# Kernel tuning notes

Hardware: AMD Instinct MI355X
Metric: run time of the kernel (lower is better)

The kernel has to match this reference:

```python
import jax, jax.numpy as jnp
import numpy as np

N_USERS = 50000
N_ITEMS = 100000
N_ENT = 200000
N_REL_TOTAL = 32  # n_relations * 2
DIM = 64
N_INTENTS = 2
N_LAYERS = 1
B = 4096
E_KG = 2_000_000
E_UI_HALF = 1_000_000  # user->item interactions; symmetrized to 2M directed edges


def setup_inputs() -> dict:
    key = jax.random.key(0)
    ks = jax.random.split(key, 16)
    s = 0.05  # xavier-ish scale
    user_emb = jax.random.normal(ks[0], (N_USERS, DIM), jnp.float32) * s
    entity_emb = jax.random.normal(ks[1], (N_ENT, DIM), jnp.float32) * s
    relation_emb = jax.random.normal(ks[2], (N_REL_TOTAL, DIM), jnp.float32) * s
    intent_weights = jax.random.normal(ks[3], (N_INTENTS, N_REL_TOTAL), jnp.float32) * s
    router_w = jax.random.normal(ks[4], (N_INTENTS, DIM), jnp.float32) * s
    router_b = jnp.zeros((N_INTENTS,), jnp.float32)
    kg_w = jax.random.normal(ks[5], (N_LAYERS, DIM, DIM), jnp.float32) * (1.0 / np.sqrt(DIM))
    item2entity = jax.random.randint(ks[6], (N_ITEMS,), 0, N_ENT)
    kg_src = jax.random.randint(ks[7], (E_KG,), 0, N_ENT)
    kg_dst = jax.random.randint(ks[8], (E_KG,), 0, N_ENT)
    kg_rel = jax.random.randint(ks[9], (E_KG,), 0, N_REL_TOTAL)
    # UI bipartite graph, symmetrically normalized (D^-1/2 A D^-1/2), as in _build_ui_graph
    rng = np.random.default_rng(0)
    uu = rng.integers(0, N_USERS, E_UI_HALF)
    ii = rng.integers(0, N_ITEMS, E_UI_HALF) + N_USERS
    rows = np.concatenate([uu, ii])
    cols = np.concatenate([ii, uu])
    n_nodes = N_USERS + N_ITEMS
    deg = np.bincount(rows, minlength=n_nodes).astype(np.float32)
    dinv = np.where(deg > 0, deg ** -0.5, 0.0).astype(np.float32)
    ui_vals = jnp.asarray(dinv[rows] * dinv[cols])
    ui_row = jnp.asarray(rows.astype(np.int32))
    ui_col = jnpseq = jnp.asarray(cols.astype(np.int32))
    u = jax.random.randint(ks[10], (B,), 0, N_USERS)
    i = jax.random.randint(ks[11], (B,), 0, N_ITEMS)
    neg_i = jax.random.randint(ks[12], (B,), 0, N_ITEMS)
    return dict(u=u, i=i, neg_i=neg_i,
                user_emb=user_emb, entity_emb=entity_emb, relation_emb=relation_emb,
                intent_weights=intent_weights, router_w=router_w, router_b=router_b,
                kg_w=kg_w, ui_vals=ui_vals,
                item2entity=item2entity, kg_src=kg_src, kg_dst=kg_dst, kg_rel=kg_rel,
                ui_row=ui_row, ui_col=ui_col)


def _l2norm(x):
    return x / jnp.maximum(jnp.linalg.norm(x, axis=-1, keepdims=True), 1e-12)


def reference(u, i, neg_i, user_emb, entity_emb, relation_emb, intent_weights,
              router_w, router_b, kg_w, ui_vals, item2entity, kg_src, kg_dst,
              kg_rel, ui_row, ui_col):
    n_ent = entity_emb.shape[0]
    # ---- _propagate_kg (dropout in eval mode = identity) ----
    x = entity_emb
    gate = jax.nn.sigmoid(relation_emb[kg_rel])  # [E, D]
    deg = jax.ops.segment_sum(jnp.ones(kg_dst.shape[0], jnp.float32), kg_dst,
                              num_segments=n_ent)
    deg = jnp.maximum(deg, 1.0)[:, None]
    for l in range(kg_w.shape[0]):
        msg = (x[kg_src] @ kg_w[l].T) * gate           # gather + linear + gate
        agg = jax.ops.segment_sum(msg, kg_dst, num_segments=n_ent)
        x = _l2norm(jax.nn.elu(agg / deg + x))
    item_kg = x[item2entity]                            # [n_items, D]
    # ---- _propagate_ui: sparse normalized adj propagation ----
    all_emb = jnp.concatenate([user_emb, item_kg], 0)
    n_nodes = all_emb.shape[0]
    embs = [all_emb]
    for _ in range(N_LAYERS):
        all_emb = jax.ops.segment_sum(ui_vals[:, None] * all_emb[ui_col], ui_row,
                                      num_segments=n_nodes)
        embs.append(all_emb)
    final = jnp.mean(jnp.stack(embs, 1), 1)
    n_users = user_emb.shape[0]
    u_prop, i_prop = final[:n_users], final[n_users:]
    # ---- intent mixing ----
    intent_dist = jax.nn.softmax(u_prop @ router_w.T + router_b, axis=-1)
    intent_emb = jax.nn.softmax(intent_weights, axis=-1) @ relation_emb
    ue = u_prop + intent_dist @ intent_emb
    ie = i_prop + item_kg
    pos = jnp.sum(ue[u] * ie[i], 1)
    neg = jnp.sum(ue[u] * ie[neg_i], 1)
    return pos, neg
```

## Files before the change

### kernel.cpp

```cpp
#include <hip/hip_runtime.h>
#include <math.h>

#define N_USERS 50000
#define N_ITEMS 100000
#define N_ENT   200000
#define N_NODES (N_USERS + N_ITEMS)
#define N_REL   32
#define DIM     64

#define NB_KG  391
#define NB_UI  586
#define NB_TOT (NB_KG + NB_UI)
#define CAPK   4096
#define CAPU   1536
#define NMMTILE 1563
#define NSCAT  768
#define NCPY   208
#define FUSE_GRID (NSCAT + NMMTILE + NCPY)

__device__ __forceinline__ unsigned short f2bf(float f) {
    unsigned u = __float_as_uint(f);
    u += 0x7FFFu + ((u >> 16) & 1u);
    return (unsigned short)(u >> 16);
}
__device__ __forceinline__ float bf_lo(unsigned v) { return __uint_as_float(v << 16); }
__device__ __forceinline__ float bf_hi(unsigned v) { return __uint_as_float(v & 0xFFFF0000u); }
__device__ __forceinline__ int getbit(const unsigned* m, int i) {
    return (m[i >> 5] >> (i & 31)) & 1;
}

__global__ __launch_bounds__(256) void build_masks(const int* __restrict__ i2e,
                                                   const int* __restrict__ u,
                                                   const int* __restrict__ ipos,
                                                   const int* __restrict__ ineg,
                                                   const float* __restrict__ rel_emb,
                                                   float2* __restrict__ gateg,
                                                   unsigned* __restrict__ ent_mask,
                                                   unsigned* __restrict__ node_mask,
                                                   int* __restrict__ bcur,
                                                   int B) {
    int t = blockIdx.x * 256 + threadIdx.x;
    int stride = gridDim.x * 256;
    for (int i = threadIdx.x; i < NB_TOT; i += 256)
        bcur[i] = (i < NB_KG) ? i * CAPK : (i - NB_KG) * CAPU;
    if (blockIdx.x == 0) {
        for (int idx = threadIdx.x; idx < N_REL * 32; idx += 256) {
            int rel = idx >> 5, hl2 = idx & 31;
            float g0 = 1.0f / (1.0f + __expf(-rel_emb[rel * 64 + 2 * hl2]));
            float g1 = 1.0f / (1.0f + __expf(-rel_emb[rel * 64 + 2 * hl2 + 1]));
            gateg[idx] = make_float2(g0, g1);
        }
    }
    for (int i = t; i < N_ITEMS; i += stride) {
        int e = i2e[i];
        atomicOr(&ent_mask[e >> 5], 1u << (e & 31));
    }
    for (int i = t; i < 3 * B; i += stride) {
        int r = (i < B) ? u[i]
              : (i < 2 * B) ? N_USERS + ipos[i - B]
                            : N_USERS + ineg[i - 2 * B];
        atomicOr(&node_mask[r >> 5], 1u << (r & 31));
    }
}

__global__ __launch_bounds__(512) void mm_scatter(const float* __restrict__ x,
                                                  const float* __restrict__ w,
                                                  unsigned short* __restrict__ y16,
                                                  int n_ent,
                                                  const int* __restrict__ kg_src,
                                                  const int* __restrict__ kg_dst,
                                                  const int* __restrict__ kg_rel,
                                                  const int* __restrict__ ui_row,
                                                  const int* __restrict__ ui_col,
                                                  const float* __restrict__ ui_vals,
                                                  const unsigned* __restrict__ ent_mask,
                                                  const unsigned* __restrict__ node_mask,
                                                  int* __restrict__ bcur,
                                                  unsigned int* __restrict__ kgrec,
                                                  int* __restrict__ uirec,
                                                  float* __restrict__ uval,
                                                  const float* __restrict__ user_emb,
                                                  unsigned short* __restrict__ all16,
                                                  int e_kg, int e_ui) {
    __shared__ __align__(16) char smem[49152];
    int tid = threadIdx.x;
    int bid = blockIdx.x;

    if (bid < NSCAT) {
        int* h     = (int*)smem;
        int* lbase = h + NB_TOT;
        int n = e_kg + e_ui;
        int nchunks = (n + 4095) >> 12;
        for (int c = bid; c < nchunks; c += NSCAT) {
            int base = c << 12;
            for (int i = tid; i < NB_TOT; i += 512) h[i] = 0;
            __syncthreads();
            unsigned int rec[8];
            float val[8];
            int bk[8];
            #pragma unroll
            for (int j = 0; j < 8; j++) {
                int e = base + j * 512 + tid;
                bk[j] = -1;
                if (e < n) {
                    if (e < e_kg) {
                        int d = kg_dst[e];
                        if (getbit(ent_mask, d)) {
                            bk[j]  = d >> 9;
                            rec[j] = (unsigned int)kg_src[e]
                                     | ((unsigned int)kg_rel[e] << 18)
                                     | ((unsigned int)(d & 511) << 23);
                            atomicAdd(&h[bk[j]], 1);
                        }
                    } else {
                        int i2 = e - e_kg;
                        int r  = ui_row[i2];
                        if (getbit(node_mask, r)) {
                            bk[j]  = NB_KG + (r >> 8);
                            rec[j] = (unsigned int)ui_col[i2]
                                     | ((unsigned int)(r & 255) << 18);
                            val[j] = ui_vals[i2];
                            atomicAdd(&h[bk[j]], 1);
                        }
                    }
                }
            }
            __syncthreads();
            for (int i = tid; i < NB_TOT; i += 512) {
                int cc = h[i];
                lbase[i] = cc ? atomicAdd(&bcur[i], cc) : 0;
            }
            __syncthreads();
            #pragma unroll
            for (int j = 0; j < 8; j++) {
                if (bk[j] >= 0) {
                    int pos = atomicAdd(&lbase[bk[j]], 1);
                    if (bk[j] < NB_KG) {
                        if (pos < (bk[j] + 1) * CAPK) kgrec[pos] = rec[j];
                    } else {
                        int bu = bk[j] - NB_KG;
                        if (pos < (bu + 1) * CAPU) { uirec[pos] = (int)rec[j]; uval[pos] = val[j]; }
                    }
                }
            }
            __syncthreads();
        }
        return;
    }

    if (bid >= NSCAT + NMMTILE) {
        int cid = bid - NSCAT - NMMTILE;
        const float4* ue4 = (const float4*)user_emb;
        uint2* a2 = (uint2*)all16;
        int total = N_USERS * 16;
        for (int i = cid * 512 + tid; i < total; i += NCPY * 512) {
            float4 v = ue4[i];
            a2[i] = make_uint2((unsigned)f2bf(v.x) | ((unsigned)f2bf(v.y) << 16),
                               (unsigned)f2bf(v.z) | ((unsigned)f2bf(v.w) << 16));
        }
        return;
    }

    int mtile = bid - NSCAT;
    float (*xt)[128] = (float (*)[128])smem;
    float (*wt)[64]  = (float (*)[64])(smem + 32768);
    int base = mtile * 128;

    #pragma unroll
    for (int q = 0; q < 2; q++) {
        int idx = q * 512 + tid;
        int j = idx >> 4, k4 = idx & 15;
        int s0 = (k4 << 2) & 28;
        float4 v = ((const float4*)w)[idx];
        wt[4 * k4 + 0][j ^ s0] = v.x;
        wt[4 * k4 + 1][j ^ s0] = v.y;
        wt[4 * k4 + 2][j ^ s0] = v.z;
        wt[4 * k4 + 3][j ^ s0] = v.w;
    }
    #pragma unroll
    for (int q = 0; q < 4; q++) {
        int idx = q * 512 + tid;
        int r = idx >> 4, k4 = idx & 15;
        int gr = base + r;
        int s0 = (k4 << 2) & 28;
        if (gr < n_ent) {
            float4 v = ((const float4*)x)[(long)gr * 16 + k4];
            xt[4 * k4 + 0][r ^ s0] = v.x;
            xt[4 * k4 + 1][r ^ s0] = v.y;
            xt[4 * k4 + 2][r ^ s0] = v.z;
            xt[4 * k4 + 3][r ^ s0] = v.w;
        }
    }
    __syncthreads();

    int j0 = (tid & 7) * 8;
    int r0 = (tid >> 3) * 2;
    float acc[2][8];
    #pragma unroll
    for (int i = 0; i < 2; i++)
        #pragma unroll
        for (int j = 0; j < 8; j++) acc[i][j] = 0.f;

    #pragma unroll 4
    for (int k = 0; k < 64; k++) {
        int s = k & 28;
        float2 xa = *(const float2*)&xt[k][r0 ^ s];
        float4 wa = *(const float4*)&wt[k][j0 ^ s];
        float4 wb = *(const float4*)&wt[k][(j0 + 4) ^ s];
        float xr[2] = {xa.x, xa.y};
        float wr[8] = {wa.x, wa.y, wa.z, wa.w, wb.x, wb.y, wb.z, wb.w};
        #pragma unroll
        for (int i = 0; i < 2; i++)
            #pragma unroll
            for (int j = 0; j < 8; j++)
                acc[i][j] += xr[i] * wr[j];
    }

    #pragma unroll
    for (int i = 0; i < 2; i++) {
        int gr = base + r0 + i;
        if (gr < n_ent) {
            uint4 o;
            o.x = (unsigned)f2bf(acc[i][0]) | ((unsigned)f2bf(acc[i][1]) << 16);
            o.y = (unsigned)f2bf(acc[i][2]) | ((unsigned)f2bf(acc[i][3]) << 16);
            o.z = (unsigned)f2bf(acc[i][4]) | ((unsigned)f2bf(acc[i][5]) << 16);
            o.w = (unsigned)f2bf(acc[i][6]) | ((unsigned)f2bf(acc[i][7]) << 16);
            *(uint4*)&y16[(long)gr * 64 + j0] = o;
        }
    }
}

__global__ __launch_bounds__(256) void bucket_finalize(const int* __restrict__ bcur,
                                                       unsigned int* __restrict__ kgrec,
                                                       int* __restrict__ uirec,
                                                       float* __restrict__ uval,
                                                       int* __restrict__ beg_kg,
                                                       int* __restrict__ end_kg,
                                                       int* __restrict__ beg_ui,
                                                       int* __restrict__ end_ui) {
    __shared__ unsigned int rec[CAPK];
    __shared__ float fval[CAPU];
    __shared__ int hist[512];
    bool iskg = blockIdx.x < NB_KG;
    int  b    = iskg ? blockIdx.x : blockIdx.x - NB_KG;
    int base  = iskg ? b * CAPK : b * CAPU;
    int cap   = iskg ? CAPK : CAPU;
    int ne    = min(bcur[blockIdx.x] - base, cap);
    int key_base = iskg ? (b << 9) : (b << 8);
    int nkeys = iskg ? min(512, N_ENT - key_base) : min(256, N_NODES - key_base);
    int SH = iskg ? 23 : 18;
    int tid = threadIdx.x;

    for (int i = tid; i < ne; i += 256) {
        if (iskg) rec[i] = kgrec[base + i];
        else { rec[i] = (unsigned int)uirec[base + i]; fval[i] = uval[base + i]; }
    }
    for (int i = tid; i < 512; i += 256) hist[i] = 0;
    __syncthreads();
    for (int i = tid; i < ne; i += 256)
        atomicAdd(&hist[rec[i] >> SH], 1);
    __syncthreads();
    int i0 = tid, i1 = tid + 256;
    int v0 = hist[i0], v1 = hist[i1];
    __syncthreads();
    for (int o = 1; o < 512; o <<= 1) {
        int a0 = (i0 >= o) ? hist[i0 - o] : 0;
        int a1 = (i1 >= o) ? hist[i1 - o] : 0;
        __syncthreads();
        hist[i0] += a0; hist[i1] += a1;
        __syncthreads();
    }
    int e0 = hist[i0] - v0, e1 = hist[i1] - v1;
    __syncthreads();
    hist[i0] = e0; hist[i1] = e1;
    int* begg = iskg ? beg_kg : beg_ui;
    int* endg = iskg ? end_kg : end_ui;
    if (i0 < nkeys) { begg[key_base + i0] = base + e0; endg[key_base + i0] = base + e0 + v0; }
    if (i1 < nkeys) { begg[key_base + i1] = base + e1; endg[key_base + i1] = base + e1 + v1; }
    __syncthreads();
    for (int i = tid; i < ne; i += 256) {
        unsigned int r = rec[i];
        int k = r >> SH;
        int slot = atomicAdd(&hist[k], 1);
        if (iskg) kgrec[base + slot] = r & 0x7FFFFFu;
        else      { uirec[base + slot] = (int)(r & 0x3FFFFu); uval[base + slot] = fval[i]; }
    }
}

__global__ __launch_bounds__(256) void kgagg_build(const int* __restrict__ beg_kg,
                                                   const int* __restrict__ end_kg,
                                                   const unsigned int* __restrict__ packed,
                                                   const unsigned short* __restrict__ y16,
                                                   const float* __restrict__ entity_emb,
                                                   const int* __restrict__ i2e,
                                                   const float4* __restrict__ gate4,
                                                   const unsigned* __restrict__ node_mask,
                                                   float* __restrict__ all_emb,
                                                   unsigned short* __restrict__ all16) {
    int lane = threadIdx.x & 63;
    int half = lane >> 5;
    int hl   = lane & 31;
    int duo  = hl >> 4;
    int ql   = hl & 15;
    long wpair = (long)((blockIdx.x * 256 + threadIdx.x) >> 6);
    int it = (int)(wpair * 2 + half);
    if (it >= N_ITEMS) return;
    int w = N_USERS + it;

    int ent = i2e[it];
    const uint2* y2 = (const uint2*)y16;
    int beg = beg_kg[ent], end = end_kg[ent];
    float a0 = 0.f, a1 = 0.f, a2 = 0.f, a3 = 0.f;
    float b0 = 0.f, b1 = 0.f, b2 = 0.f, b3 = 0.f;
    int p = beg;
    for (; p + 4 <= end; p += 4) {
        unsigned pk0 = packed[p + duo];
        unsigned pk1 = packed[p + 2 + duo];
        uint2 v0 = y2[(long)(pk0 & 0x3FFFF) * 16 + ql];
        uint2 v1 = y2[(long)(pk1 & 0x3FFFF) * 16 + ql];
        float4 g0 = gate4[(pk0 >> 18) * 16 + ql];
        float4 g1 = gate4[(pk1 >> 18) * 16 + ql];
        a0 += bf_lo(v0.x) * g0.x;  a1 += bf_hi(v0.x) * g0.y;
        a2 += bf_lo(v0.y) * g0.z;  a3 += bf_hi(v0.y) * g0.w;
        b0 += bf_lo(v1.x) * g1.x;  b1 += bf_hi(v1.x) * g1.y;
        b2 += bf_lo(v1.y) * g1.z;  b3 += bf_hi(v1.y) * g1.w;
    }
    if (p + duo < end) {
        unsigned pk = packed[p + duo];
        uint2 v = y2[(long)(pk & 0x3FFFF) * 16 + ql];
        float4 g = gate4[(pk >> 18) * 16 + ql];
        a0 += bf_lo(v.x) * g.x;  a1 += bf_hi(v.x) * g.y;
        a2 += bf_lo(v.y) * g.z;  a3 += bf_hi(v.y) * g.w;
    }
    if (p + 2 + duo < end) {
        unsigned pk = packed[p + 2 + duo];
        uint2 v = y2[(long)(pk & 0x3FFFF) * 16 + ql];
        float4 g = gate4[(pk >> 18) * 16 + ql];
        b0 += bf_lo(v.x) * g.x;  b1 += bf_hi(v.x) * g.y;
        b2 += bf_lo(v.y) * g.z;  b3 += bf_hi(v.y) * g.w;
    }
    a0 += b0; a1 += b1; a2 += b2; a3 += b3;
    a0 += __shfl_xor(a0, 16);
    a1 += __shfl_xor(a1, 16);
    a2 += __shfl_xor(a2, 16);
    a3 += __shfl_xor(a3, 16);

    float deg = fmaxf((float)(end - beg), 1.0f);
    float4 xv = ((const float4*)entity_emb)[(long)ent * 16 + ql];
    float v0 = a0 / deg + xv.x;
    float v1 = a1 / deg + xv.y;
    float v2 = a2 / deg + xv.z;
    float v3 = a3 / deg + xv.w;
    v0 = (v0 > 0.0f) ? v0 : (__expf(v0) - 1.0f);
    v1 = (v1 > 0.0f) ? v1 : (__expf(v1) - 1.0f);
    v2 = (v2 > 0.0f) ? v2 : (__expf(v2) - 1.0f);
    v3 = (v3 > 0.0f) ? v3 : (__expf(v3) - 1.0f);
    float ss = v0 * v0 + v1 * v1 + v2 * v2 + v3 * v3;
    ss += __shfl_xor(ss, 1);
    ss += __shfl_xor(ss, 2);
    ss += __shfl_xor(ss, 4);
    ss += __shfl_xor(ss, 8);
    float inv = 1.0f / fmaxf(sqrtf(ss), 1e-12f);
    if (duo == 0) {
        float r0 = v0 * inv, r1 = v1 * inv, r2 = v2 * inv, r3 = v3 * inv;
        if (getbit(node_mask, w))
            ((float4*)all_emb)[(long)w * 16 + ql] = make_float4(r0, r1, r2, r3);
        ((uint2*)all16)[(long)w * 16 + ql] =
            make_uint2((unsigned)f2bf(r0) | ((unsigned)f2bf(r1) << 16),
                       (unsigned)f2bf(r2) | ((unsigned)f2bf(r3) << 16));
    }
}

__global__ __launch_bounds__(256) void ui_aggregate_s(const int* __restrict__ beg_ui,
                                                      const int* __restrict__ end_ui,
                                                      const int* __restrict__ colrec,
                                                      const float* __restrict__ uval,
                                                      const float* __restrict__ all_emb,
                                                      const float* __restrict__ user_emb,
                                                      const unsigned short* __restrict__ all16,
                                                      const int* __restrict__ u,
                                                      const int* __restrict__ ipos,
                                                      const int* __restrict__ ineg,
                                                      float* __restrict__ final_emb, int B) {
    const uint2* a2p = (const uint2*)all16;
    int lane = threadIdx.x & 63;
    int half = lane >> 5;
    int hl   = lane & 31;
    int duo  = hl >> 4;
    int ql   = hl & 15;
    long wpair = (long)((blockIdx.x * 256 + threadIdx.x) >> 6);
    int s = (int)(wpair * 2 + half);
    if (s >= 3 * B) return;
    int r;
    if (s < B)          r = u[s];
    else if (s < 2 * B) r = N_USERS + ipos[s - B];
    else                r = N_USERS + ineg[s - 2 * B];

    int beg = beg_ui[r], end = end_ui[r];
    float a0 = 0.f, a1 = 0.f, a2 = 0.f, a3 = 0.f;
    float b0 = 0.f, b1 = 0.f, b2 = 0.f, b3 = 0.f;
    int p = beg;
    for (; p + 4 <= end; p += 4) {
        int   c0 = colrec[p + duo];
        int   c1 = colrec[p + 2 + duo];
        float d0 = uval[p + duo];
        float d1 = uval[p + 2 + duo];
        uint2 v0 = a2p[(long)c0 * 16 + ql];
        uint2 v1 = a2p[(long)c1 * 16 + ql];
        a0 += d0 * bf_lo(v0.x);  a1 += d0 * bf_hi(v0.x);
        a2 += d0 * bf_lo(v0.y);  a3 += d0 * bf_hi(v0.y);
        b0 += d1 * bf_lo(v1.x);  b1 += d1 * bf_hi(v1.x);
        b2 += d1 * bf_lo(v1.y);  b3 += d1 * bf_hi(v1.y);
    }
    if (p + duo < end) {
        int   c = colrec[p + duo];
        float d = uval[p + duo];
        uint2 v = a2p[(long)c * 16 + ql];
        a0 += d * bf_lo(v.x);  a1 += d * bf_hi(v.x);
        a2 += d * bf_lo(v.y);  a3 += d * bf_hi(v.y);
    }
    if (p + 2 + duo < end) {
        int   c = colrec[p + 2 + duo];
        float d = uval[p + 2 + duo];
        uint2 v = a2p[(long)c * 16 + ql];
        b0 += d * bf_lo(v.x);  b1 += d * bf_hi(v.x);
        b2 += d * bf_lo(v.y);  b3 += d * bf_hi(v.y);
    }
    a0 += b0; a1 += b1; a2 += b2; a3 += b3;
    a0 += __shfl_xor(a0, 16);
    a1 += __shfl_xor(a1, 16);
    a2 += __shfl_xor(a2, 16);
    a3 += __shfl_xor(a3, 16);
    if (duo == 0) {
        float4 ae = (r < N_USERS)
            ? ((const float4*)user_emb)[(long)r * 16 + ql]
            : ((const float4*)all_emb)[(long)r * 16 + ql];
        ((float4*)final_emb)[(long)r * 16 + ql] =
            make_float4(0.5f * (ae.x + a0), 0.5f * (ae.y + a1),
                        0.5f * (ae.z + a2), 0.5f * (ae.w + a3));
    }
}

__global__ void final_kernel(const int* __restrict__ u, const int* __restrict__ ipos,
                             const int* __restrict__ ineg,
                             const float* __restrict__ final_emb,
                             const float* __restrict__ all_emb,
                             const float* __restrict__ rw, const float* __restrict__ rb,
                             const float* __restrict__ iw, const float* __restrict__ rel_emb,
                             float* __restrict__ out, int B) {
    __shared__ float sh_intent[128];
    if (threadIdx.x < 64) {
        int j = threadIdx.x;
        for (int k = 0; k < 2; k++) {
            float m = -1e30f;
            for (int r = 0; r < N_REL; r++) m = fmaxf(m, iw[k * N_REL + r]);
            float Z = 0.f, acc = 0.f;
            for (int r = 0; r < N_REL; r++) {
                float e = __expf(iw[k * N_REL + r] - m);
                Z += e;
                acc += e * rel_emb[r * 64 + j];
            }
            sh_intent[k * 64 + j] = acc / Z;
        }
    }
    __syncthreads();
    int lane = threadIdx.x & 63;
    int wave = (blockIdx.x * blockDim.x + threadIdx.x) >> 6;
    int nw   = (gridDim.x * blockDim.x) >> 6;
    for (int b = wave; b < B; b += nw) {
        int uu = u[b];
        float up = final_emb[(long)uu * 64 + lane];
        float l0 = up * rw[lane];
        float l1 = up * rw[64 + lane];
        #pragma unroll
        for (int o = 32; o; o >>= 1) {
            l0 += __shfl_xor(l0, o);
            l1 += __shfl_xor(l1, o);
        }
        l0 += rb[0]; l1 += rb[1];
        float m  = fmaxf(l0, l1);
        float e0 = __expf(l0 - m), e1 = __expf(l1 - m);
        float inv = 1.0f / (e0 + e1);
        float p0 = e0 * inv, p1 = e1 * inv;
        float ue = up + p0 * sh_intent[lane] + p1 * sh_intent[64 + lane];

        int it = ipos[b];
        long rr = (long)(N_USERS + it) * 64 + lane;
        float ie = final_emb[rr] + all_emb[rr];
        float dp = ue * ie;
        #pragma unroll
        for (int o = 32; o; o >>= 1) dp += __shfl_xor(dp, o);
        if (lane == 0) out[b] = dp;

        it = ineg[b];
        rr = (long)(N_USERS + it) * 64 + lane;
        ie = final_emb[rr] + all_emb[rr];
        dp = ue * ie;
        #pragma unroll
        for (int o = 32; o; o >>= 1) dp += __shfl_xor(dp, o);
        if (lane == 0) out[B + b] = dp;
    }
}

extern "C" void kernel_launch(void* const* d_in, const int* in_sizes, int n_in,
                              void* d_out, int out_size, void* d_ws, size_t ws_size,
                              hipStream_t stream) {
    const int*   u          = (const int*)  d_in[0];
    const int*   ipos       = (const int*)  d_in[1];
    const int*   ineg       = (const int*)  d_in[2];
    const float* user_emb   = (const float*)d_in[3];
    const float* entity_emb = (const float*)d_in[4];
    const float* rel_emb    = (const float*)d_in[5];
    const float* iw         = (const float*)d_in[6];
    const float* rw         = (const float*)d_in[7];
    const float* rb         = (const float*)d_in[8];
    const float* kgw        = (const float*)d_in[9];
    const float* ui_vals    = (const float*)d_in[10];
    const int*   i2e        = (const int*)  d_in[11];
    const int*   kg_src     = (const int*)  d_in[12];
    const int*   kg_dst     = (const int*)  d_in[13];
    const int*   kg_rel     = (const int*)  d_in[14];
    const int*   ui_row     = (const int*)  d_in[15];
    const int*   ui_col     = (const int*)  d_in[16];
    float*       out        = (float*)d_out;

    int B    = in_sizes[0];
    int e_kg = in_sizes[12];
    int e_ui = in_sizes[15];

    char* ws = (char*)d_ws;
    unsigned short* y16       = (unsigned short*)(ws + 0);
    float*          all_emb   = (float*)(ws + 25600000);
    unsigned short* all16     = (unsigned short*)(ws + 64000000);
    float*          final_emb = (float*)(ws + 83200000);
    unsigned int*   kgrec     = (unsigned int*)(ws + 121600000);
    int*            end_kg    = (int*)(ws + 128006144);
    int*            end_ui    = (int*)(ws + 128806144);
    int*            uirec     = (int*)(ws + 129600000);
    float*          uval      = (float*)(ws + 133600000);
    int*            beg_kg    = (int*)(ws + 137600000);
    int*            beg_ui    = (int*)(ws + 138400256);
    unsigned*       ent_mask  = (unsigned*)(ws + 139000512);
    unsigned*       node_mask = (unsigned*)(ws + 139025600);
    int*            bcur      = (int*)(ws + 139608704);
    float2*         gateg     = (float2*)(ws + 139612672);

    hipMemsetAsync(ent_mask, 0, 25088 + 18752, stream);
    build_masks<<<512, 256, 0, stream>>>(i2e, u, ipos, ineg, rel_emb, gateg,
                                         ent_mask, node_mask, bcur, B);
    mm_scatter <<<FUSE_GRID, 512, 0, stream>>>(
        entity_emb, kgw, y16, N_ENT,
        kg_src, kg_dst, kg_rel, ui_row, ui_col, ui_vals,
        ent_mask, node_mask, bcur, kgrec, uirec, uval,
        user_emb, all16, e_kg, e_ui);
    bucket_finalize<<<NB_TOT, 256, 0, stream>>>(bcur, kgrec, uirec, uval,
                                                beg_kg, end_kg, beg_ui, end_ui);
    {
        int nwaves = N_ITEMS / 2;
        int nblk   = (nwaves * 64 + 255) / 256;
        kgagg_build<<<nblk, 256, 0, stream>>>(
            beg_kg, end_kg, kgrec, y16, entity_emb, i2e,
            (const float4*)gateg, node_mask, all_emb, all16);
    }
    {
        int nwaves = (3 * B + 1) / 2;
        int nblk   = (nwaves * 64 + 255) / 256;
        ui_aggregate_s<<<nblk, 256, 0, stream>>>(
            beg_ui, end_ui, uirec, uval, all_emb, user_emb, all16,
            u, ipos, ineg, final_emb, B);
    }
    final_kernel<<<256, 256, 0, stream>>>(u, ipos, ineg, final_emb, all_emb,
                                          rw, rb, iw, rel_emb, out, B);
}
```

Baseline: 273.1 us.

## Use 16 lanes per row in aggregation kernels; move user bf16 copy to finalize

The KG and UI aggregation kernels now give each row 16 lanes instead of 32, packing four rows per wavefront. Each lane walks every edge with four independent accumulators rather than splitting edges across two half-groups and reducing with shuffles. This halves the wave count, drops the cross-half shuffle reduction and keeps all lanes active on the store, at the cost of more serial gathers per lane. Separately, the fp32-to-bf16 copy of user embeddings moves from the large fused mm/scatter kernel into extra blocks of the bucket-finalize kernel, shrinking the fused grid.

```diff
diff --git a/kernel.cpp b/kernel.cpp
--- a/kernel.cpp
+++ b/kernel.cpp
@@ -15,8 +15,8 @@
 #define CAPU   1536
 #define NMMTILE 1563
 #define NSCAT  768
+#define FUSE_GRID (NSCAT + NMMTILE)
 #define NCPY   208
-#define FUSE_GRID (NSCAT + NMMTILE + NCPY)
 
 __device__ __forceinline__ unsigned short f2bf(float f) {
     unsigned u = __float_as_uint(f);
@@ -79,8 +79,6 @@
                                                   unsigned int* __restrict__ kgrec,
                                                   int* __restrict__ uirec,
                                                   float* __restrict__ uval,
-                                                  const float* __restrict__ user_emb,
-                                                  unsigned short* __restrict__ all16,
                                                   int e_kg, int e_ui) {
     __shared__ __align__(16) char smem[49152];
     int tid = threadIdx.x;
@@ -148,19 +146,6 @@
         return;
     }
 
-    if (bid >= NSCAT + NMMTILE) {
-        int cid = bid - NSCAT - NMMTILE;
-        const float4* ue4 = (const float4*)user_emb;
-        uint2* a2 = (uint2*)all16;
-        int total = N_USERS * 16;
-        for (int i = cid * 512 + tid; i < total; i += NCPY * 512) {
-            float4 v = ue4[i];
-            a2[i] = make_uint2((unsigned)f2bf(v.x) | ((unsigned)f2bf(v.y) << 16),
-                               (unsigned)f2bf(v.z) | ((unsigned)f2bf(v.w) << 16));
-        }
-        return;
-    }
-
     int mtile = bid - NSCAT;
     float (*xt)[128] = (float (*)[128])smem;
     float (*wt)[64]  = (float (*)[64])(smem + 32768);
@@ -237,10 +222,27 @@
                                                        int* __restrict__ beg_kg,
                                                        int* __restrict__ end_kg,
                                                        int* __restrict__ beg_ui,
-                                                       int* __restrict__ end_ui) {
+                                                       int* __restrict__ end_ui,
+                                                       const float* __restrict__ user_emb,
+                                                       unsigned short* __restrict__ all16) {
     __shared__ unsigned int rec[CAPK];
     __shared__ float fval[CAPU];
     __shared__ int hist[512];
+    int tid = threadIdx.x;
+
+    if (blockIdx.x >= NB_TOT) {
+        int cid = blockIdx.x - NB_TOT;
+        const float4* ue4 = (const float4*)user_emb;
+        uint2* a2 = (uint2*)all16;
+        int total = N_USERS * 16;
+        for (int i = cid * 256 + tid; i < total; i += NCPY * 256) {
+            float4 v = ue4[i];
+            a2[i] = make_uint2((unsigned)f2bf(v.x) | ((unsigned)f2bf(v.y) << 16),
+                               (unsigned)f2bf(v.z) | ((unsigned)f2bf(v.w) << 16));
+        }
+        return;
+    }
+
     bool iskg = blockIdx.x < NB_KG;
     int  b    = iskg ? blockIdx.x : blockIdx.x - NB_KG;
     int base  = iskg ? b * CAPK : b * CAPU;
@@ -249,7 +251,6 @@
     int key_base = iskg ? (b << 9) : (b << 8);
     int nkeys = iskg ? min(512, N_ENT - key_base) : min(256, N_NODES - key_base);
     int SH = iskg ? 23 : 18;
-    int tid = threadIdx.x;
 
     for (int i = tid; i < ne; i += 256) {
         if (iskg) rec[i] = kgrec[base + i];
@@ -298,12 +299,10 @@
                                                    float* __restrict__ all_emb,
                                                    unsigned short* __restrict__ all16) {
     int lane = threadIdx.x & 63;
-    int half = lane >> 5;
-    int hl   = lane & 31;
-    int duo  = hl >> 4;
-    int ql   = hl & 15;
-    long wpair = (long)((blockIdx.x * 256 + threadIdx.x) >> 6);
-    int it = (int)(wpair * 2 + half);
+    int q4   = lane >> 4;
+    int ql   = lane & 15;
+    long wq = (long)((blockIdx.x * 256 + threadIdx.x) >> 6);
+    int it = (int)(wq * 4 + q4);
     if (it >= N_ITEMS) return;
     int w = N_USERS + it;
 
@@ -312,45 +311,63 @@
     int beg = beg_kg[ent], end = end_kg[ent];
     float a0 = 0.f, a1 = 0.f, a2 = 0.f, a3 = 0.f;
     float b0 = 0.f, b1 = 0.f, b2 = 0.f, b3 = 0.f;
+    float c0 = 0.f, c1 = 0.f, c2 = 0.f, c3 = 0.f;
+    float d0 = 0.f, d1 = 0.f, d2 = 0.f, d3 = 0.f;
     int p = beg;
     for (; p + 4 <= end; p += 4) {
-        unsigned pk0 = packed[p + duo];
-        unsigned pk1 = packed[p + 2 + duo];
+        unsigned pk0 = packed[p + 0];
+        unsigned pk1 = packed[p + 1];
+        unsigned pk2 = packed[p + 2];
+        unsigned pk3 = packed[p + 3];
         uint2 v0 = y2[(long)(pk0 & 0x3FFFF) * 16 + ql];
         uint2 v1 = y2[(long)(pk1 & 0x3FFFF) * 16 + ql];
+        uint2 v2 = y2[(long)(pk2 & 0x3FFFF) * 16 + ql];
+        uint2 v3 = y2[(long)(pk3 & 0x3FFFF) * 16 + ql];
         float4 g0 = gate4[(pk0 >> 18) * 16 + ql];
         float4 g1 = gate4[(pk1 >> 18) * 16 + ql];
+        float4 g2 = gate4[(pk2 >> 18) * 16 + ql];
+        float4 g3 = gate4[(pk3 >> 18) * 16 + ql];
         a0 += bf_lo(v0.x) * g0.x;  a1 += bf_hi(v0.x) * g0.y;
         a2 += bf_lo(v0.y) * g0.z;  a3 += bf_hi(v0.y) * g0.w;
         b0 += bf_lo(v1.x) * g1.x;  b1 += bf_hi(v1.x) * g1.y;
         b2 += bf_lo(v1.y) * g1.z;  b3 += bf_hi(v1.y) * g1.w;
-    }
-    if (p + duo < end) {
-        unsigned pk = packed[p + duo];
+        c0 += bf_lo(v2.x) * g2.x;  c1 += bf_hi(v2.x) * g2.y;
+        c2 += bf_lo(v2.y) * g2.z;  c3 += bf_hi(v2.y) * g2.w;
+        d0 += bf_lo(v3.x) * g3.x;  d1 += bf_hi(v3.x) * g3.y;
+        d2 += bf_lo(v3.y) * g3.z;  d3 += bf_hi(v3.y) * g3.w;
+    }
+    if (p < end) {
+        unsigned pk = packed[p];
         uint2 v = y2[(long)(pk & 0x3FFFF) * 16 + ql];
         float4 g = gate4[(pk >> 18) * 16 + ql];
         a0 += bf_lo(v.x) * g.x;  a1 += bf_hi(v.x) * g.y;
         a2 += bf_lo(v.y) * g.z;  a3 += bf_hi(v.y) * g.w;
     }
-    if (p + 2 + duo < end) {
-        unsigned pk = packed[p + 2 + duo];
+    if (p + 1 < end) {
+        unsigned pk = packed[p + 1];
         uint2 v = y2[(long)(pk & 0x3FFFF) * 16 + ql];
         float4 g = gate4[(pk >> 18) * 16 + ql];
         b0 += bf_lo(v.x) * g.x;  b1 += bf_hi(v.x) * g.y;
         b2 += bf_lo(v.y) * g.z;  b3 += bf_hi(v.y) * g.w;
     }
-    a0 += b0; a1 += b1; a2 += b2; a3 += b3;
-    a0 += __shfl_xor(a0, 16);
-    a1 += __shfl_xor(a1, 16);
-    a2 += __shfl_xor(a2, 16);
-    a3 += __shfl_xor(a3, 16);
+    if (p + 2 < end) {
+        unsigned pk = packed[p + 2];
+        uint2 v = y2[(long)(pk & 0x3FFFF) * 16 + ql];
+        float4 g = gate4[(pk >> 18) * 16 + ql];
+        c0 += bf_lo(v.x) * g.x;  c1 += bf_hi(v.x) * g.y;
+        c2 += bf_lo(v.y) * g.z;  c3 += bf_hi(v.y) * g.w;
+    }
+    float s0 = (a0 + b0) + (c0 + d0);
+    float s1 = (a1 + b1) + (c1 + d1);
+    float s2 = (a2 + b2) + (c2 + d2);
+    float s3 = (a3 + b3) + (c3 + d3);
 
     float deg = fmaxf((float)(end - beg), 1.0f);
     float4 xv = ((const float4*)entity_emb)[(long)ent * 16 + ql];
-    float v0 = a0 / deg + xv.x;
-    float v1 = a1 / deg + xv.y;
-    float v2 = a2 / deg + xv.z;
-    float v3 = a3 / deg + xv.w;
+    float v0 = s0 / deg + xv.x;
+    float v1 = s1 / deg + xv.y;
+    float v2 = s2 / deg + xv.z;
+    float v3 = s3 / deg + xv.w;
     v0 = (v0 > 0.0f) ? v0 : (__expf(v0) - 1.0f);
     v1 = (v1 > 0.0f) ? v1 : (__expf(v1) - 1.0f);
     v2 = (v2 > 0.0f) ? v2 : (__expf(v2) - 1.0f);
@@ -361,14 +378,12 @@
     ss += __shfl_xor(ss, 4);
     ss += __shfl_xor(ss, 8);
     float inv = 1.0f / fmaxf(sqrtf(ss), 1e-12f);
-    if (duo == 0) {
-        float r0 = v0 * inv, r1 = v1 * inv, r2 = v2 * inv, r3 = v3 * inv;
-        if (getbit(node_mask, w))
-            ((float4*)all_emb)[(long)w * 16 + ql] = make_float4(r0, r1, r2, r3);
-        ((uint2*)all16)[(long)w * 16 + ql] =
-            make_uint2((unsigned)f2bf(r0) | ((unsigned)f2bf(r1) << 16),
-                       (unsigned)f2bf(r2) | ((unsigned)f2bf(r3) << 16));
-    }
+    float r0 = v0 * inv, r1 = v1 * inv, r2 = v2 * inv, r3 = v3 * inv;
+    if (getbit(node_mask, w))
+        ((float4*)all_emb)[(long)w * 16 + ql] = make_float4(r0, r1, r2, r3);
+    ((uint2*)all16)[(long)w * 16 + ql] =
+        make_uint2((unsigned)f2bf(r0) | ((unsigned)f2bf(r1) << 16),
+                   (unsigned)f2bf(r2) | ((unsigned)f2bf(r3) << 16));
 }
 
 __global__ __launch_bounds__(256) void ui_aggregate_s(const int* __restrict__ beg_ui,
@@ -384,12 +399,10 @@
                                                       float* __restrict__ final_emb, int B) {
     const uint2* a2p = (const uint2*)all16;
     int lane = threadIdx.x & 63;
-    int half = lane >> 5;
-    int hl   = lane & 31;
-    int duo  = hl >> 4;
-    int ql   = hl & 15;
-    long wpair = (long)((blockIdx.x * 256 + threadIdx.x) >> 6);
-    int s = (int)(wpair * 2 + half);
+    int q4   = lane >> 4;
+    int ql   = lane & 15;
+    long wq = (long)((blockIdx.x * 256 + threadIdx.x) >> 6);
+    int s = (int)(wq * 4 + q4);
     if (s >= 3 * B) return;
     int r;
     if (s < B)          r = u[s];
@@ -399,46 +412,59 @@
     int beg = beg_ui[r], end = end_ui[r];
     float a0 = 0.f, a1 = 0.f, a2 = 0.f, a3 = 0.f;
     float b0 = 0.f, b1 = 0.f, b2 = 0.f, b3 = 0.f;
+    float c0 = 0.f, c1 = 0.f, c2 = 0.f, c3 = 0.f;
+    float d0 = 0.f, d1 = 0.f, d2 = 0.f, d3 = 0.f;
     int p = beg;
     for (; p + 4 <= end; p += 4) {
-        int   c0 = colrec[p + duo];
-        int   c1 = colrec[p + 2 + duo];
-        float d0 = uval[p + duo];
-        float d1 = uval[p + 2 + duo];
-        uint2 v0 = a2p[(long)c0 * 16 + ql];
-        uint2 v1 = a2p[(long)c1 * 16 + ql];
-        a0 += d0 * bf_lo(v0.x);  a1 += d0 * bf_hi(v0.x);
-        a2 += d0 * bf_lo(v0.y);  a3 += d0 * bf_hi(v0.y);
-        b0 += d1 * bf_lo(v1.x);  b1 += d1 * bf_hi(v1.x);
-        b2 += d1 * bf_lo(v1.y);  b3 += d1 * bf_hi(v1.y);
-    }
-    if (p + duo < end) {
-        int   c = colrec[p + duo];
-        float d = uval[p + duo];
-        uint2 v = a2p[(long)c * 16 + ql];
-        a0 += d * bf_lo(v.x);  a1 += d * bf_hi(v.x);
-        a2 += d * bf_lo(v.y);  a3 += d * bf_hi(v.y);
-    }
-    if (p + 2 + duo < end) {
-        int   c = colrec[p + 2 + duo];
-        float d = uval[p + 2 + duo];
-        uint2 v = a2p[(long)c * 16 + ql];
-        b0 += d * bf_lo(v.x);  b1 += d * bf_hi(v.x);
-        b2 += d * bf_lo(v.y);  b3 += d * bf_hi(v.y);
-    }
-    a0 += b0; a1 += b1; a2 += b2; a3 += b3;
-    a0 += __shfl_xor(a0, 16);
-    a1 += __shfl_xor(a1, 16);
-    a2 += __shfl_xor(a2, 16);
-    a3 += __shfl_xor(a3, 16);
-    if (duo == 0) {
-        float4 ae = (r < N_USERS)
-            ? ((const float4*)user_emb)[(long)r * 16 + ql]
-            : ((const float4*)all_emb)[(long)r * 16 + ql];
-        ((float4*)final_emb)[(long)r * 16 + ql] =
-            make_float4(0.5f * (ae.x + a0), 0.5f * (ae.y + a1),
-                        0.5f * (ae.z + a2), 0.5f * (ae.w + a3));
-    }
+        int   cc0 = colrec[p + 0];
+        int   cc1 = colrec[p + 1];
+        int   cc2 = colrec[p + 2];
+        int   cc3 = colrec[p + 3];
+        float w0 = uval[p + 0];
+        float w1 = uval[p + 1];
+        float w2 = uval[p + 2];
+        float w3 = uval[p + 3];
+        uint2 v0 = a2p[(long)cc0 * 16 + ql];
+        uint2 v1 = a2p[(long)cc1 * 16 + ql];
+        uint2 v2 = a2p[(long)cc2 * 16 + ql];
+        uint2 v3 = a2p[(long)cc3 * 16 + ql];
+        a0 += w0 * bf_lo(v0.x);  a1 += w0 * bf_hi(v0.x);
+        a2 += w0 * bf_lo(v0.y);  a3 += w0 * bf_hi(v0.y);
+        b0 += w1 * bf_lo(v1.x);  b1 += w1 * bf_hi(v1.x);
+        b2 += w1 * bf_lo(v1.y);  b3 += w1 * bf_hi(v1.y);
+        c0 += w2 * bf_lo(v2.x);  c1 += w2 * bf_hi(v2.x);
+        c2 += w2 * bf_lo(v2.y);  c3 += w2 * bf_hi(v2.y);
+        d0 += w3 * bf_lo(v3.x);  d1 += w3 * bf_hi(v3.x);
+        d2 += w3 * bf_lo(v3.y);  d3 += w3 * bf_hi(v3.y);
+    }
+    if (p < end) {
+        int cc = colrec[p]; float wv = uval[p];
+        uint2 v = a2p[(long)cc * 16 + ql];
+        a0 += wv * bf_lo(v.x);  a1 += wv * bf_hi(v.x);
+        a2 += wv * bf_lo(v.y);  a3 += wv * bf_hi(v.y);
+    }
+    if (p + 1 < end) {
+        int cc = colrec[p + 1]; float wv = uval[p + 1];
+        uint2 v = a2p[(long)cc * 16 + ql];
+        b0 += wv * bf_lo(v.x);  b1 += wv * bf_hi(v.x);
+        b2 += wv * bf_lo(v.y);  b3 += wv * bf_hi(v.y);
+    }
+    if (p + 2 < end) {
+        int cc = colrec[p + 2]; float wv = uval[p + 2];
+        uint2 v = a2p[(long)cc * 16 + ql];
+        c0 += wv * bf_lo(v.x);  c1 += wv * bf_hi(v.x);
+        c2 += wv * bf_lo(v.y);  c3 += wv * bf_hi(v.y);
+    }
+    float s0 = (a0 + b0) + (c0 + d0);
+    float s1 = (a1 + b1) + (c1 + d1);
+    float s2 = (a2 + b2) + (c2 + d2);
+    float s3 = (a3 + b3) + (c3 + d3);
+    float4 ae = (r < N_USERS)
+        ? ((const float4*)user_emb)[(long)r * 16 + ql]
+        : ((const float4*)all_emb)[(long)r * 16 + ql];
+    ((float4*)final_emb)[(long)r * 16 + ql] =
+        make_float4(0.5f * (ae.x + s0), 0.5f * (ae.y + s1),
+                    0.5f * (ae.z + s2), 0.5f * (ae.w + s3));
 }
 
 __global__ void final_kernel(const int* __restrict__ u, const int* __restrict__ ipos,
@@ -551,19 +577,19 @@
     mm_scatter <<<FUSE_GRID, 512, 0, stream>>>(
         entity_emb, kgw, y16, N_ENT,
         kg_src, kg_dst, kg_rel, ui_row, ui_col, ui_vals,
-        ent_mask, node_mask, bcur, kgrec, uirec, uval,
-        user_emb, all16, e_kg, e_ui);
-    bucket_finalize<<<NB_TOT, 256, 0, stream>>>(bcur, kgrec, uirec, uval,
-                                                beg_kg, end_kg, beg_ui, end_ui);
+        ent_mask, node_mask, bcur, kgrec, uirec, uval, e_kg, e_ui);
+    bucket_finalize<<<NB_TOT + NCPY, 256, 0, stream>>>(bcur, kgrec, uirec, uval,
+                                                       beg_kg, end_kg, beg_ui, end_ui,
+                                                       user_emb, all16);
     {
-        int nwaves = N_ITEMS / 2;
+        int nwaves = N_ITEMS / 4;
         int nblk   = (nwaves * 64 + 255) / 256;
         kgagg_build<<<nblk, 256, 0, stream>>>(
             beg_kg, end_kg, kgrec, y16, entity_emb, i2e,
             (const float4*)gateg, node_mask, all_emb, all16);
     }
     {
-        int nwaves = (3 * B + 1) / 2;
+        int nwaves = (3 * B + 3) / 4;
         int nblk   = (nwaves * 64 + 255) / 256;
         ui_aggregate_s<<<nblk, 256, 0, stream>>>(
             beg_ui, end_ui, uirec, uval, all_emb, user_emb, all16,
```

Measured after the change: 274.6 us. Within noise of the previous version (+0.5%).
